# Optimization experiments

Hardware: AMD Instinct MI355X
Metric: run time of the kernel (lower is better)

Reference implementation:

```python
import jax, jax.numpy as jnp
import numpy as np

STRIDE = 1

def setup_inputs() -> dict:
    key = jax.random.key(0)
    k1, k2, k3 = jax.random.split(key, 3)
    x = jax.random.normal(k1, (32, 64, 112, 112), dtype=jnp.float32)
    weight = jax.random.normal(k2, (128, 64, 3, 3), dtype=jnp.float32)
    bias = jax.random.normal(k3, (128,), dtype=jnp.float32)
    return {"x": x, "weight": weight, "bias": bias}

def reference(x, weight, bias):
    # Naive per-patch multiply-sum conv == standard cross-correlation conv2d,
    # stride=1, no padding (VALID).  x: (N,Cin,H,W), weight: (Cout,Cin,kH,kW)
    out = jax.lax.conv_general_dilated(
        x, weight,
        window_strides=(STRIDE, STRIDE),
        padding="VALID",
        dimension_numbers=("NCHW", "OIHW", "NCHW"),
    )
    return out + bias[None, :, None, None]
```

## Files before the change

kernel.cpp:

```cpp
#include <hip/hip_runtime.h>
#include <hip/hip_bf16.h>


#define CIN   64
#define COUT  128
#define INH   112
#define INW   112
#define OUTH  110
#define OUTW  110
#define NB    32
#define KTOT  576
#define NPIX  (NB*OUTH*OUTW)

typedef __attribute__((ext_vector_type(8))) short short8;
typedef __attribute__((ext_vector_type(4))) float f32x4;
typedef __attribute__((ext_vector_type(4))) unsigned int uint4v;

static __device__ __forceinline__ unsigned short f2bf(float f) {
    union { float f; unsigned int u; } v; v.f = f;
    return (unsigned short)((v.u + 0x7FFF + ((v.u >> 16) & 1)) >> 16);
}

__global__ __launch_bounds__(256) void convert_x(const float* __restrict__ x,
                                                 unsigned short* __restrict__ xhwc) {
    __shared__ unsigned short lds[64 * 117];
    const int h = blockIdx.x;
    const int n = blockIdx.y;
    const int t = threadIdx.x;
    const float* xp = x + ((size_t)n * CIN) * (INH * INW) + (size_t)h * INW;
#pragma unroll
    for (int i = 0; i < 28; ++i) {
        int f = t + 256 * i;
        int ci = f / 112, w = f - ci * 112;
        lds[ci * 117 + w] = f2bf(xp[(size_t)ci * (INH * INW) + w]);
    }
    __syncthreads();
    unsigned int* dst = (unsigned int*)(xhwc + ((size_t)(n * INH + h) * INW) * 64);
#pragma unroll
    for (int i = 0; i < 14; ++i) {
        int g = t + 256 * i;
        int w = g >> 5, cp = g & 31;
        unsigned int lo = lds[(cp * 2) * 117 + w];
        unsigned int hi = lds[(cp * 2 + 1) * 117 + w];
        dst[g] = lo | (hi << 16);
    }
}

__global__ __launch_bounds__(256) void prepack_w(const float* __restrict__ w,
                                                 unsigned short* __restrict__ ap) {
    int flat = blockIdx.x * 256 + threadIdx.x;
    int m = flat / KTOT;
    int k = flat - m * KTOT;
    int khw = k >> 6, ci = k & 63;
    int kh = khw / 3, kw = khw - kh * 3;
    float v = w[((m * CIN + ci) * 3 + kh) * 3 + kw];
    ap[((k >> 3) * COUT + m) * 8 + (k & 7)] = f2bf(v);
}

__global__ __launch_bounds__(256) void conv_gemm(const unsigned short* __restrict__ xhwc,
                                                 const unsigned short* __restrict__ ap,
                                                 const float* __restrict__ bias,
                                                 float* __restrict__ out) {
    __shared__ unsigned short ldsB[25600];
    const int oh = blockIdx.x;
    const int n  = blockIdx.y;
    const int t  = threadIdx.x;

    {
        const uint4v* src = (const uint4v*)(xhwc + ((size_t)(n * INH + oh) * INW) * 64);
        for (int c = t; c < 2688; c += 256) {
            int kh = c / 896;
            int r  = c - kh * 896;
            int w_ = r >> 3, part = r & 7;
            *(uint4v*)&ldsB[(kh * INW + w_) * 72 + part * 8] = src[c];
        }
    }
    __syncthreads();

    const int lane = t & 63;
    const int wave = t >> 6;
    const int m_base  = (wave >> 1) * 64;
    const int px_base = (wave & 1) * 64;
    const int l16  = lane & 15;
    const int quad = lane >> 4;

    f32x4 acc[4][4] = {};
    const short8* A = (const short8*)ap;

    for (int kc = 0; kc < 18; ++kc) {
        const int khw = kc >> 1;
        const int kh = khw / 3, kw = khw - kh * 3;
        const int ci0 = (kc & 1) * 32 + quad * 8;
        short8 a[4], b[4];
#pragma unroll
        for (int i = 0; i < 4; ++i)
            a[i] = A[(kc * 4 + quad) * COUT + (m_base + i * 16 + l16)];
#pragma unroll
        for (int j = 0; j < 4; ++j) {
            int ow = px_base + j * 16 + l16;
            b[j] = *(const short8*)&ldsB[(kh * INW + ow + kw) * 72 + ci0];
        }
#pragma unroll
        for (int i = 0; i < 4; ++i)
#pragma unroll
            for (int j = 0; j < 4; ++j)
                acc[i][j] = __builtin_amdgcn_mfma_f32_16x16x32_bf16(a[i], b[j], acc[i][j], 0, 0, 0);
    }

#pragma unroll
    for (int i = 0; i < 4; ++i) {
        const int co = m_base + i * 16 + quad * 4;
#pragma unroll
        for (int j = 0; j < 4; ++j) {
            const int ow = px_base + j * 16 + l16;
            if (ow < OUTW) {
                const size_t ob = (((size_t)n * COUT + co) * OUTH + oh) * OUTW + ow;
#pragma unroll
                for (int r = 0; r < 4; ++r)
                    out[ob + (size_t)r * (OUTH * OUTW)] = acc[i][j][r] + bias[co + r];
            }
        }
    }
}

#define TCO 16
__global__ __launch_bounds__(256) void conv_direct(const float* __restrict__ x,
                                                   const float* __restrict__ w,
                                                   const float* __restrict__ bias,
                                                   float* __restrict__ out) {
    int p = blockIdx.x * 256 + threadIdx.x;
    const int co0 = blockIdx.y * TCO;
    const bool valid = p < NPIX;
    if (!valid) p = 0;
    const int n = p / (OUTH * OUTW);
    const int rem = p - n * (OUTH * OUTW);
    const int oh = rem / OUTW;
    const int ow = rem - oh * OUTW;
    float acc[TCO];
#pragma unroll
    for (int t = 0; t < TCO; ++t) acc[t] = bias[co0 + t];
    const float* xb = x + ((size_t)n * CIN) * (INH * INW) + (size_t)oh * INW + ow;
    const float* wb = w + (size_t)co0 * CIN * 9;
    for (int ci = 0; ci < CIN; ++ci) {
        const float* xp = xb + (size_t)ci * (INH * INW);
        const float* wp = wb + ci * 9;
#pragma unroll
        for (int kh = 0; kh < 3; ++kh) {
            const float x0 = xp[kh * INW + 0];
            const float x1 = xp[kh * INW + 1];
            const float x2 = xp[kh * INW + 2];
#pragma unroll
            for (int t = 0; t < TCO; ++t) {
                const float* wt = wp + t * (CIN * 9) + kh * 3;
                acc[t] = fmaf(x0, wt[0], acc[t]);
                acc[t] = fmaf(x1, wt[1], acc[t]);
                acc[t] = fmaf(x2, wt[2], acc[t]);
            }
        }
    }
    if (valid) {
        const size_t ob = ((size_t)n * COUT + co0) * (OUTH * OUTW) + (size_t)oh * OUTW + ow;
#pragma unroll
        for (int t = 0; t < TCO; ++t)
            out[ob + (size_t)t * (OUTH * OUTW)] = acc[t];
    }
}

extern "C" void kernel_launch(void* const* d_in, const int* in_sizes, int n_in,
                              void* d_out, int out_size, void* d_ws, size_t ws_size,
                              hipStream_t stream) {
    const float* x    = (const float*)d_in[0];
    const float* w    = (const float*)d_in[1];
    const float* bias = (const float*)d_in[2];
    float* out        = (float*)d_out;

    const size_t xhwc_bytes = (size_t)NB * INH * INW * 64 * 2;
    const size_t ap_bytes   = (size_t)COUT * KTOT * 2;

    if (ws_size >= xhwc_bytes + ap_bytes) {
        unsigned short* xhwc = (unsigned short*)d_ws;
        unsigned short* apck = (unsigned short*)((char*)d_ws + xhwc_bytes);
        convert_x<<<dim3(INH, NB), 256, 0, stream>>>(x, xhwc);
        prepack_w<<<288, 256, 0, stream>>>(w, apck);
        conv_gemm<<<dim3(OUTH, NB), 256, 0, stream>>>(xhwc, apck, bias, out);
    } else {
        dim3 grid((NPIX + 255) / 256, COUT / TCO);
        conv_direct<<<grid, dim3(256), 0, stream>>>(x, w, bias, out);
    }
}
```

Before: 370.0 us.

## Double-buffer operand loads in conv GEMM and simplify NHWC conversion

The conv_gemm inner K loop is fully unrolled and double-buffered so the next chunk's A (global) and B (LDS) fragments load while the current MFMAs run. Launch bounds request 3 blocks per SM, and the bias is read as a vector load. convert_x drops its LDS transpose: each thread gathers 8 channels per pixel straight from global memory and writes a packed 16-byte bf16 vector. The extra buffered registers under the occupancy bound may raise register pressure or cause spills, and the new convert gather reads with a large channel stride.

```diff
diff --git a/kernel.cpp b/kernel.cpp
--- a/kernel.cpp
+++ b/kernel.cpp
@@ -20,29 +20,25 @@
     union { float f; unsigned int u; } v; v.f = f;
     return (unsigned short)((v.u + 0x7FFF + ((v.u >> 16) & 1)) >> 16);
 }
+static __device__ __forceinline__ unsigned int pack2(float lo, float hi) {
+    return (unsigned int)f2bf(lo) | ((unsigned int)f2bf(hi) << 16);
+}
 
 __global__ __launch_bounds__(256) void convert_x(const float* __restrict__ x,
                                                  unsigned short* __restrict__ xhwc) {
-    __shared__ unsigned short lds[64 * 117];
     const int h = blockIdx.x;
     const int n = blockIdx.y;
-    const int t = threadIdx.x;
     const float* xp = x + ((size_t)n * CIN) * (INH * INW) + (size_t)h * INW;
+    unsigned int* dst = (unsigned int*)(xhwc + ((size_t)(n * INH + h) * INW) * 64);
+    for (int c = threadIdx.x; c < 896; c += 256) {
+        const int w = c >> 3, grp = c & 7;
+        float v[8];
 #pragma unroll
-    for (int i = 0; i < 28; ++i) {
-        int f = t + 256 * i;
-        int ci = f / 112, w = f - ci * 112;
-        lds[ci * 117 + w] = f2bf(xp[(size_t)ci * (INH * INW) + w]);
-    }
-    __syncthreads();
-    unsigned int* dst = (unsigned int*)(xhwc + ((size_t)(n * INH + h) * INW) * 64);
-#pragma unroll
-    for (int i = 0; i < 14; ++i) {
-        int g = t + 256 * i;
-        int w = g >> 5, cp = g & 31;
-        unsigned int lo = lds[(cp * 2) * 117 + w];
-        unsigned int hi = lds[(cp * 2 + 1) * 117 + w];
-        dst[g] = lo | (hi << 16);
+        for (int j = 0; j < 8; ++j)
+            v[j] = xp[(size_t)(grp * 8 + j) * (INH * INW) + w];
+        uint4v o = { pack2(v[0], v[1]), pack2(v[2], v[3]),
+                     pack2(v[4], v[5]), pack2(v[6], v[7]) };
+        *(uint4v*)&dst[(w * 64 + grp * 8) >> 1] = o;
     }
 }
 
@@ -57,10 +53,10 @@
     ap[((k >> 3) * COUT + m) * 8 + (k & 7)] = f2bf(v);
 }
 
-__global__ __launch_bounds__(256) void conv_gemm(const unsigned short* __restrict__ xhwc,
-                                                 const unsigned short* __restrict__ ap,
-                                                 const float* __restrict__ bias,
-                                                 float* __restrict__ out) {
+__global__ __launch_bounds__(256, 3) void conv_gemm(const unsigned short* __restrict__ xhwc,
+                                                    const unsigned short* __restrict__ ap,
+                                                    const float* __restrict__ bias,
+                                                    float* __restrict__ out) {
     __shared__ unsigned short ldsB[25600];
     const int oh = blockIdx.x;
     const int n  = blockIdx.y;
@@ -84,40 +80,51 @@
     const int l16  = lane & 15;
     const int quad = lane >> 4;
 
+    int pxw[4];
+#pragma unroll
+    for (int j = 0; j < 4; ++j) pxw[j] = px_base + j * 16 + l16;
+
     f32x4 acc[4][4] = {};
     const short8* A = (const short8*)ap;
 
-    for (int kc = 0; kc < 18; ++kc) {
+    short8 abuf[2][4], bbuf[2][4];
+    auto loadf = [&](int kc, short8* aa, short8* bb) {
         const int khw = kc >> 1;
         const int kh = khw / 3, kw = khw - kh * 3;
         const int ci0 = (kc & 1) * 32 + quad * 8;
-        short8 a[4], b[4];
 #pragma unroll
         for (int i = 0; i < 4; ++i)
-            a[i] = A[(kc * 4 + quad) * COUT + (m_base + i * 16 + l16)];
+            aa[i] = A[(kc * 4 + quad) * COUT + (m_base + i * 16 + l16)];
 #pragma unroll
-        for (int j = 0; j < 4; ++j) {
-            int ow = px_base + j * 16 + l16;
-            b[j] = *(const short8*)&ldsB[(kh * INW + ow + kw) * 72 + ci0];
-        }
+        for (int j = 0; j < 4; ++j)
+            bb[j] = *(const short8*)&ldsB[(kh * INW + pxw[j] + kw) * 72 + ci0];
+    };
+
+    loadf(0, abuf[0], bbuf[0]);
+#pragma unroll
+    for (int kc = 0; kc < 18; ++kc) {
+        const int cur = kc & 1;
+        if (kc < 17) loadf(kc + 1, abuf[cur ^ 1], bbuf[cur ^ 1]);
 #pragma unroll
         for (int i = 0; i < 4; ++i)
 #pragma unroll
             for (int j = 0; j < 4; ++j)
-                acc[i][j] = __builtin_amdgcn_mfma_f32_16x16x32_bf16(a[i], b[j], acc[i][j], 0, 0, 0);
+                acc[i][j] = __builtin_amdgcn_mfma_f32_16x16x32_bf16(
+                    abuf[cur][i], bbuf[cur][j], acc[i][j], 0, 0, 0);
     }
 
 #pragma unroll
     for (int i = 0; i < 4; ++i) {
         const int co = m_base + i * 16 + quad * 4;
+        const f32x4 bv = *(const f32x4*)&bias[co];
 #pragma unroll
         for (int j = 0; j < 4; ++j) {
-            const int ow = px_base + j * 16 + l16;
+            const int ow = pxw[j];
             if (ow < OUTW) {
                 const size_t ob = (((size_t)n * COUT + co) * OUTH + oh) * OUTW + ow;
 #pragma unroll
                 for (int r = 0; r < 4; ++r)
-                    out[ob + (size_t)r * (OUTH * OUTW)] = acc[i][j][r] + bias[co + r];
+                    out[ob + (size_t)r * (OUTH * OUTW)] = acc[i][j][r] + bv[r];
             }
         }
     }
```

New measurement: 374.0 us. About the same (+1.1%).
